# Kernel tuning notes

Measured on AMD Instinct MI355X. Metric: run time of the kernel, lower is better.

Reference implementation:

```python
import jax, jax.numpy as jnp
import numpy as np

B, N, K, NS = 2, 1024, 64, 32          # batch, points, keypoints (top-k), ball-query neighbors
RADIUS = 1.0                            # ball-query radius (sample_and_group)
R_VOX, S_VOX = 2.0, 0.4                 # voxelize search radius / step
NV = int(round(2 * R_VOX / S_VOX)) + 1  # 11 offsets per axis
C = NV ** 3                             # 1331 candidates per keypoint
F = 32                                  # deep feature channels (num_feat)


def _gather(data, idx):
    # data: (B, N, ...) ; idx: (B, ...) int -> (B, idx_shape..., ...)
    return jax.vmap(lambda d, i: d[i])(data, idx)


def setup_inputs() -> dict:
    key = jax.random.key(0)
    ks = jax.random.split(key, 16)
    f = lambda k, s: jax.random.normal(k, s, dtype=jnp.float32)
    return {
        "src_pts": f(ks[0], (B, 6, N)),
        "tgt_pts": f(ks[1], (B, 6, N)),
        "R_init": f(ks[2], (1, 3, 3)),
        "t_init": f(ks[3], (3, 1)),
        # feature-extraction shared MLP (6 -> 32 -> 32)
        "W1": f(ks[4], (6, F)) * 0.4, "b1": jnp.zeros((F,), jnp.float32),
        "W2": f(ks[5], (F, F)) * 0.2, "b2": jnp.zeros((F,), jnp.float32),
        # weighting (saliency) MLP (32 -> 16 -> 1)
        "Ww1": f(ks[6], (F, 16)) * 0.3, "bw1": jnp.zeros((16,), jnp.float32),
        "Ww2": f(ks[7], (16, 1)) * 0.3, "bw2": jnp.zeros((1,), jnp.float32),
        # deep-feature-embedding shared MLP (3+32 -> 32 -> 32)
        "Wd1": f(ks[8], (3 + F, F)) * 0.3, "bd1": jnp.zeros((F,), jnp.float32),
        "Wd2": f(ks[9], (F, F)) * 0.2, "bd2": jnp.zeros((F,), jnp.float32),
    }


def reference(src_pts, tgt_pts, R_init, t_init,
              W1, b1, W2, b2, Ww1, bw1, Ww2, bw2, Wd1, bd1, Wd2, bd2):
    def fe(pts):                                   # shared feature extraction (FE1)
        x = jnp.transpose(pts, (0, 2, 1))          # (B,N,6)
        h = jax.nn.relu(x @ W1 + b1)
        return x[..., :3], jax.nn.relu(h @ W2 + b2)  # xyz (B,N,3), feat (B,N,F)

    def dfe(x):                                    # shared DFE mini-PointNet MLP
        h = jax.nn.relu(x @ Wd1 + bd1)
        return jax.nn.relu(h @ Wd2 + bd2)

    src_xyz_all, src_feat = fe(src_pts)
    tgt_xyz_all, tgt_feat = fe(tgt_pts)

    # ---- weighting layer: per-point saliency, top-K keypoints ----
    score = (jax.nn.relu(src_feat @ Ww1 + bw1) @ Ww2 + bw2)[..., 0]  # (B,N)
    _, key_idx = jax.lax.top_k(score, K)                              # (B,K)

    src_pts_T = jnp.transpose(src_pts, (0, 2, 1))                     # (B,N,6)
    keypts = _gather(src_pts_T, key_idx)                              # (B,K,6)
    kxyz = keypts[..., :3]                                            # (B,K,3)

    # ---- sample_and_group: ball query among keypoints (npoint == K) ----
    sqd = jnp.sum((kxyz[:, :, None] - kxyz[:, None]) ** 2, -1)        # (B,K,K)
    gidx = jnp.broadcast_to(jnp.arange(K), (B, K, K))
    gidx = jnp.where(sqd > RADIUS ** 2, K, gidx)
    gidx = jnp.sort(gidx, -1)[:, :, :NS]
    gidx = jnp.where(gidx == K, gidx[:, :, :1], gidx)                 # (B,K,NS)

    grouped = _gather(kxyz, gidx)                                     # (B,K,NS,3)
    rel = grouped - kxyz[:, :, None]                                  # local coords
    orig_idx = _gather(key_idx, gidx)                                 # (B,K,NS) into N
    keyfeats = _gather(src_feat, orig_idx)                            # (B,K,NS,F)
    src_cat = jnp.concatenate([rel, keyfeats], -1)                    # (B,K,NS,3+F)

    # ---- voxelize: candidate grid around R_init-transformed keypoints ----
    Rm = jnp.broadcast_to(R_init, (B, 3, 3))
    kxyz_t = jnp.einsum('bij,bkj->bki', Rm, kxyz)                     # (B,K,3)
    off = jnp.linspace(-R_VOX, R_VOX, NV, dtype=jnp.float32)
    gx, gy, gz = jnp.meshgrid(off, off, off, indexing='ij')
    grid = jnp.stack([gx, gy, gz], -1).reshape(-1, 3)                 # (C,3)
    cand = kxyz_t[:, :, None, :] + grid                               # (B,K,C,3)

    # ---- 1-NN of each candidate in the target cloud (feature lookup) ----
    cn = jnp.sum(cand ** 2, -1)                                       # (B,K,C)
    tn = jnp.sum(tgt_xyz_all ** 2, -1)                                # (B,N)
    cross = jnp.einsum('bkcd,bnd->bkcn', cand, tgt_xyz_all)           # (B,K,C,N)
    d = cn[..., None] + tn[:, None, None, :] - 2.0 * cross
    nn = jnp.argmin(jax.lax.stop_gradient(d), -1)                     # (B,K,C)
    nn_xyz = _gather(tgt_xyz_all, nn)                                 # (B,K,C,3)
    nn_feat = _gather(tgt_feat, nn)                                   # (B,K,C,F)
    tgt_cat = jnp.concatenate([cand - nn_xyz, nn_feat], -1)           # (B,K,C,3+F)

    # ---- DFE embeddings + corresponding-point generation (CPG) ----
    src_emb = jnp.max(dfe(src_cat), axis=2)                           # (B,K,F)  max over neighbors
    tgt_emb = dfe(tgt_cat)                                            # (B,K,C,F)
    sim = jnp.einsum('bkd,bkcd->bkc', src_emb, tgt_emb)               # (B,K,C)
    w = jax.nn.softmax(sim, -1)
    tgt_vcp = jnp.einsum('bkc,bkcd->bkd', w, cand)                    # (B,K,3)

    return kxyz, tgt_vcp
```

## Files before the change

kernel.cpp:

```cpp
#include <hip/hip_runtime.h>
#include <math.h>

#define BB 2
#define NPTS 1024
#define KK 64
#define NSZ 32
#define CC 1331
#define FF 32
#define RAD2 1.0f
#define NCOL 121
#define NRNG 8

__global__ __launch_bounds__(64)
void k_features(const float* __restrict__ src_pts, const float* __restrict__ tgt_pts,
                const float* __restrict__ W1, const float* __restrict__ b1,
                const float* __restrict__ W2, const float* __restrict__ b2,
                const float* __restrict__ Ww1, const float* __restrict__ bw1,
                const float* __restrict__ Ww2, const float* __restrict__ bw2,
                const float* __restrict__ Wd1, const float* __restrict__ bd1,
                float* __restrict__ src_feat, float* __restrict__ tgt_A,
                float* __restrict__ tgt_m2, float* __restrict__ score)
{
    int gid = blockIdx.x * blockDim.x + threadIdx.x;
    int isTgt = gid >= BB * NPTS;
    int pn = gid & (BB * NPTS - 1);
    int b = pn >> 10, n = pn & 1023;
    const float* pts = isTgt ? tgt_pts : src_pts;
    float p[6];
#pragma unroll
    for (int i = 0; i < 6; i++) p[i] = pts[(b * 6 + i) * NPTS + n];
    float h[FF];
#pragma unroll
    for (int j = 0; j < FF; j++) {
        float a = b1[j];
#pragma unroll
        for (int i = 0; i < 6; i++) a = fmaf(p[i], W1[i * FF + j], a);
        h[j] = fmaxf(a, 0.0f);
    }
    float ft[FF];
#pragma unroll
    for (int j = 0; j < FF; j++) {
        float a = b2[j];
#pragma unroll
        for (int i = 0; i < FF; i++) a = fmaf(h[i], W2[i * FF + j], a);
        ft[j] = fmaxf(a, 0.0f);
    }
    if (isTgt) {
        float x = p[0], y = p[1], z = p[2];
        float4 v; v.x = x; v.y = y; v.z = z; v.w = x * x + y * y + z * z;
        ((float4*)tgt_m2)[b * NPTS + n] = v;
        float av[FF];
#pragma unroll
        for (int j = 0; j < FF; j++) av[j] = bd1[j];
#pragma unroll
        for (int i = 0; i < FF; i++) {
            float fi = ft[i];
#pragma unroll
            for (int j = 0; j < FF; j++)
                av[j] = fmaf(fi, Wd1[(3 + i) * FF + j], av[j]);
        }
#pragma unroll
        for (int j = 0; j < FF; j++) tgt_A[(b * NPTS + n) * FF + j] = av[j];
    } else {
#pragma unroll
        for (int j = 0; j < FF; j++) src_feat[(b * NPTS + n) * FF + j] = ft[j];
        float acc = bw2[0];
#pragma unroll
        for (int j = 0; j < 16; j++) {
            float a = bw1[j];
#pragma unroll
            for (int i = 0; i < FF; i++) a = fmaf(ft[i], Ww1[i * 16 + j], a);
            acc = fmaf(fmaxf(a, 0.0f), Ww2[j], acc);
        }
        score[b * NPTS + n] = acc;
    }
}

__global__ __launch_bounds__(256)
void k_rank(const float* __restrict__ score, const float* __restrict__ src_pts,
            const float* __restrict__ R,
            int* __restrict__ key_idx, float* __restrict__ kxyz,
            float* __restrict__ kxyz_t, float* __restrict__ out_kxyz)
{
    int blk = blockIdx.x;
    int b = blk >> 4;
    int pbase = (blk & 15) << 6;
    int t = threadIdx.x;
    int sub = t & 3;
    int lp = t >> 2;
    int n = pbase + lp;
    __shared__ float sc[NPTS];
    for (int i = t; i < NPTS; i += 256) sc[i] = score[b * NPTS + i];
    __syncthreads();
    float s = sc[n];
    int rank = 0;
#pragma unroll 8
    for (int jj = 0; jj < 256; jj++) {
        int j = (jj << 2) | sub;
        float sj = sc[j];
        bool before = (sj > s) || (sj == s && j < n);
        rank += before ? 1 : 0;
    }
    rank += __shfl_xor(rank, 1, 64);
    rank += __shfl_xor(rank, 2, 64);
    if (sub == 0 && rank < KK) {
        key_idx[b * KK + rank] = n;
        float x = src_pts[(b * 6 + 0) * NPTS + n];
        float y = src_pts[(b * 6 + 1) * NPTS + n];
        float z = src_pts[(b * 6 + 2) * NPTS + n];
        int o = (b * KK + rank) * 3;
        kxyz[o] = x; kxyz[o + 1] = y; kxyz[o + 2] = z;
        out_kxyz[o] = x; out_kxyz[o + 1] = y; out_kxyz[o + 2] = z;
#pragma unroll
        for (int i = 0; i < 3; i++)
            kxyz_t[o + i] = R[i * 3 + 0] * x + R[i * 3 + 1] * y + R[i * 3 + 2] * z;
    }
}

__global__ __launch_bounds__(64)
void k_group_emb(const float* __restrict__ kxyz, const int* __restrict__ key_idx,
                 const float* __restrict__ src_feat,
                 const float* __restrict__ Wd1, const float* __restrict__ bd1,
                 const float* __restrict__ Wd2, const float* __restrict__ bd2,
                 float* __restrict__ src_emb)
{
    int b = blockIdx.x / KK, kk = blockIdx.x % KK;
    int t = threadIdx.x;
    __shared__ float kx[KK][3];
    __shared__ float emb[NSZ][FF];
    kx[t][0] = kxyz[(b * KK + t) * 3 + 0];
    kx[t][1] = kxyz[(b * KK + t) * 3 + 1];
    kx[t][2] = kxyz[(b * KK + t) * 3 + 2];
    __syncthreads();
    float cx = kx[kk][0], cy = kx[kk][1], cz = kx[kk][2];
    float dx = kx[t][0] - cx, dy = kx[t][1] - cy, dz = kx[t][2] - cz;
    float sq = dx * dx + dy * dy + dz * dz;
    unsigned long long mask = __ballot(sq <= RAD2);
    if (t < NSZ) {
        int cnt = __popcll(mask);
        int want = (t < cnt) ? t : 0;
        unsigned long long mm = mask;
        for (int q = 0; q < want; q++) mm &= (mm - 1);
        int g = __ffsll(mm) - 1;
        float xr = kx[g][0] - cx, yr = kx[g][1] - cy, zr = kx[g][2] - cz;
        int orig = key_idx[b * KK + g];
        const float* fz = &src_feat[(b * NPTS + orig) * FF];
        float fr[FF];
#pragma unroll
        for (int i = 0; i < FF; i++) fr[i] = fz[i];
        float h[FF];
#pragma unroll
        for (int j = 0; j < FF; j++) {
            float a = bd1[j];
            a = fmaf(xr, Wd1[0 * FF + j], a);
            a = fmaf(yr, Wd1[1 * FF + j], a);
            a = fmaf(zr, Wd1[2 * FF + j], a);
#pragma unroll
            for (int i = 0; i < FF; i++) a = fmaf(fr[i], Wd1[(3 + i) * FF + j], a);
            h[j] = fmaxf(a, 0.0f);
        }
#pragma unroll
        for (int j = 0; j < FF; j++) {
            float a = bd2[j];
#pragma unroll
            for (int i = 0; i < FF; i++) a = fmaf(h[i], Wd2[i * FF + j], a);
            emb[t][j] = fmaxf(a, 0.0f);
        }
    }
    __syncthreads();
    if (t < FF) {
        float m = emb[0][t];
#pragma unroll
        for (int s2 = 1; s2 < NSZ; s2++) m = fmaxf(m, emb[s2][t]);
        src_emb[(b * KK + kk) * FF + t] = m;
    }
}

__global__ __launch_bounds__(256)
void k_scan(const float* __restrict__ kxyz_t, const float* __restrict__ tgt_m2,
            float2* __restrict__ part)
{
    int bid = blockIdx.x;
    int bk = bid >> 3, r = bid & 7;
    int b = bk >> 6;
    int t = threadIdx.x;
    int u = t >> 7, lt = t & 127;
    __shared__ float4 P[128];
    __shared__ float2 pbuf[2][NCOL][11];
    if (t < 128) P[t] = ((const float4*)tgt_m2)[(b << 10) + (r << 7) + t];
    float kx = kxyz_t[bk * 3 + 0], ky = kxyz_t[bk * 3 + 1], kz = kxyz_t[bk * 3 + 2];
    float kx2 = -2.0f * kx, ky2 = -2.0f * ky, kz2 = -2.0f * kz;
    int p = lt;
    bool active = p < NCOL;
    int pc = active ? p : 0;
    int ixv = pc / 11, iyv = pc - ixv * 11;
    float gx2 = -2.0f * (-2.0f + ixv * 0.4f);
    float gy2 = -2.0f * (-2.0f + iyv * 0.4f);
    float gz2[11];
#pragma unroll
    for (int iz = 0; iz < 11; iz++) gz2[iz] = -2.0f * (-2.0f + iz * 0.4f);
    float best[11]; int bn[11];
#pragma unroll
    for (int iz = 0; iz < 11; iz++) { best[iz] = 3.0e38f; bn[iz] = 0; }
    __syncthreads();
    if (active) {
        const int pb = u << 6;
#pragma unroll 8
        for (int i = 0; i < 64; i++) {
            float4 v = P[pb + i];
            float a = fmaf(kx2, v.x, fmaf(ky2, v.y, fmaf(kz2, v.z, v.w)));
            float e = fmaf(gx2, v.x, fmaf(gy2, v.y, a));
#pragma unroll
            for (int iz = 0; iz < 11; iz++) {
                float d = fmaf(gz2[iz], v.z, e);
                bool l = d < best[iz];
                best[iz] = l ? d : best[iz];
                bn[iz] = l ? i : bn[iz];
            }
        }
#pragma unroll
        for (int iz = 0; iz < 11; iz++)
            pbuf[u][p][iz] = make_float2(best[iz], __int_as_float(bn[iz] + (u << 6)));
    }
    __syncthreads();
    if (u == 0 && active) {
        int cbase = ((bk << 3) + r) * CC + p * 11;
#pragma unroll
        for (int iz = 0; iz < 11; iz++) {
            float2 r0 = pbuf[0][p][iz], r1 = pbuf[1][p][iz];
            float2 m = (r1.x < r0.x) ? r1 : r0;
            part[cbase + iz] = make_float2(m.x,
                __int_as_float(__float_as_int(m.y) + (r << 7)));
        }
    }
}

__global__ __launch_bounds__(256)
void k_mlp(const float2* __restrict__ part, const float* __restrict__ kxyz_t,
           const float* __restrict__ tgt_m2, const float* __restrict__ tgt_A,
           const float* __restrict__ src_emb,
           const float* __restrict__ Wd1,
           const float* __restrict__ Wd2, const float* __restrict__ bd2,
           float* __restrict__ sim)
{
    const int NCH = 6;
    int bid = blockIdx.x;
    int chunk = bid % NCH;
    int bk = bid / NCH;
    int b = bk >> 6;
    int t = threadIdx.x;
    int c = chunk * 256 + t;
    int cc = min(c, CC - 1);
    float2 rb = part[(bk << 3) * CC + cc];
#pragma unroll
    for (int r = 1; r < NRNG; r++) {
        float2 o = part[((bk << 3) + r) * CC + cc];
        if (o.x < rb.x) rb = o;
    }
    int nb = __float_as_int(rb.y);
    float4 nv = ((const float4*)tgt_m2)[(b << 10) + nb];
    const float4* az = (const float4*)&tgt_A[((b << 10) + nb) * FF];
    float h[FF];
#pragma unroll
    for (int i = 0; i < FF / 4; i++) {
        float4 v = az[i];
        h[i * 4 + 0] = v.x; h[i * 4 + 1] = v.y; h[i * 4 + 2] = v.z; h[i * 4 + 3] = v.w;
    }
    int ixv = cc / 121, rem = cc - ixv * 121, iyv = rem / 11, izv = rem - iyv * 11;
    float cx = kxyz_t[bk * 3 + 0] + (-2.0f + ixv * 0.4f);
    float cy = kxyz_t[bk * 3 + 1] + (-2.0f + iyv * 0.4f);
    float cz = kxyz_t[bk * 3 + 2] + (-2.0f + izv * 0.4f);
    float x0 = cx - nv.x, x1 = cy - nv.y, x2 = cz - nv.z;
#pragma unroll
    for (int j = 0; j < FF; j++) {
        float a = h[j];
        a = fmaf(x0, Wd1[0 * FF + j], a);
        a = fmaf(x1, Wd1[1 * FF + j], a);
        a = fmaf(x2, Wd1[2 * FF + j], a);
        h[j] = fmaxf(a, 0.0f);
    }
    float sv = 0.0f;
#pragma unroll
    for (int j = 0; j < FF; j++) {
        float a = bd2[j];
#pragma unroll
        for (int i = 0; i < FF; i++) a = fmaf(h[i], Wd2[i * FF + j], a);
        sv = fmaf(fmaxf(a, 0.0f), src_emb[bk * FF + j], sv);
    }
    if (c < CC) sim[bk * CC + c] = sv;
}

__global__ __launch_bounds__(256)
void k_softmax(const float* __restrict__ sim, const float* __restrict__ kxyz_t,
               float* __restrict__ out_vcp)
{
    int bk = blockIdx.x;
    int t = threadIdx.x;
    __shared__ float red[256];
    __shared__ float4 red4[256];
    float kx = kxyz_t[bk * 3 + 0], ky = kxyz_t[bk * 3 + 1], kz = kxyz_t[bk * 3 + 2];
    float lm = -3.0e38f;
    for (int c = t; c < CC; c += 256) lm = fmaxf(lm, sim[bk * CC + c]);
    red[t] = lm;
    __syncthreads();
    for (int s2 = 128; s2 > 0; s2 >>= 1) {
        if (t < s2) red[t] = fmaxf(red[t], red[t + s2]);
        __syncthreads();
    }
    float m = red[0];
    float se = 0.f, sx = 0.f, sy = 0.f, sz = 0.f;
    for (int c = t; c < CC; c += 256) {
        float e = expf(sim[bk * CC + c] - m);
        int ix = c / 121, rem = c - ix * 121, iy = rem / 11, iz = rem - iy * 11;
        float cxx = kx + (-2.0f + ix * 0.4f);
        float cyy = ky + (-2.0f + iy * 0.4f);
        float czz = kz + (-2.0f + iz * 0.4f);
        se += e;
        sx = fmaf(e, cxx, sx);
        sy = fmaf(e, cyy, sy);
        sz = fmaf(e, czz, sz);
    }
    red4[t] = make_float4(se, sx, sy, sz);
    __syncthreads();
    for (int s2 = 128; s2 > 0; s2 >>= 1) {
        if (t < s2) {
            float4 a = red4[t], bq = red4[t + s2];
            red4[t] = make_float4(a.x + bq.x, a.y + bq.y, a.z + bq.z, a.w + bq.w);
        }
        __syncthreads();
    }
    if (t == 0) {
        float4 r = red4[0];
        out_vcp[bk * 3 + 0] = r.y / r.x;
        out_vcp[bk * 3 + 1] = r.z / r.x;
        out_vcp[bk * 3 + 2] = r.w / r.x;
    }
}

extern "C" void kernel_launch(void* const* d_in, const int* in_sizes, int n_in,
                              void* d_out, int out_size, void* d_ws, size_t ws_size,
                              hipStream_t stream)
{
    (void)in_sizes; (void)n_in; (void)out_size; (void)ws_size;
    const float* src_pts = (const float*)d_in[0];
    const float* tgt_pts = (const float*)d_in[1];
    const float* R_init  = (const float*)d_in[2];
    const float* W1  = (const float*)d_in[4];
    const float* b1  = (const float*)d_in[5];
    const float* W2  = (const float*)d_in[6];
    const float* b2  = (const float*)d_in[7];
    const float* Ww1 = (const float*)d_in[8];
    const float* bw1 = (const float*)d_in[9];
    const float* Ww2 = (const float*)d_in[10];
    const float* bw2 = (const float*)d_in[11];
    const float* Wd1 = (const float*)d_in[12];
    const float* bd1 = (const float*)d_in[13];
    const float* Wd2 = (const float*)d_in[14];
    const float* bd2 = (const float*)d_in[15];

    float* ws = (float*)d_ws;
    float* src_feat = ws;
    float* tgt_A    = src_feat + BB * NPTS * FF;
    float* tgt_m2   = tgt_A + BB * NPTS * FF;
    float* score    = tgt_m2 + BB * NPTS * 4;
    int*   key_idx  = (int*)(score + BB * NPTS);
    float* kxyz     = (float*)(key_idx + BB * KK);
    float* kxyz_t   = kxyz + BB * KK * 3;
    float* src_emb  = kxyz_t + BB * KK * 3;
    float* sim      = src_emb + BB * KK * FF;
    float2* part    = (float2*)(sim + BB * KK * CC);

    float* out_kxyz = (float*)d_out;
    float* out_vcp  = out_kxyz + BB * KK * 3;

    k_features<<<64, 64, 0, stream>>>(
        src_pts, tgt_pts, W1, b1, W2, b2, Ww1, bw1, Ww2, bw2, Wd1, bd1,
        src_feat, tgt_A, tgt_m2, score);
    k_rank<<<BB * 16, 256, 0, stream>>>(score, src_pts, R_init,
                                        key_idx, kxyz, kxyz_t, out_kxyz);
    k_group_emb<<<BB * KK, 64, 0, stream>>>(kxyz, key_idx, src_feat,
                                            Wd1, bd1, Wd2, bd2, src_emb);
    k_scan<<<BB * KK * NRNG, 256, 0, stream>>>(kxyz_t, tgt_m2, part);
    k_mlp<<<BB * KK * 6, 256, 0, stream>>>(part, kxyz_t, tgt_m2, tgt_A, src_emb,
                                           Wd1, Wd2, bd2, sim);
    k_softmax<<<BB * KK, 256, 0, stream>>>(sim, kxyz_t, out_vcp);
}
```

Baseline: 74.97 us.

## Fuse all stages into one persistent kernel with global atomic barriers

Replaces six kernel launches with a single 256-block persistent kernel that runs each stage in turn, separated by atomic-counter grid barriers. The barrier counter is reset with a memset before launch. The goal is to remove per-launch overhead and the gaps between the small dependent kernels. The scan stage is also reorganised: each block now handles half the target ranges in four passes over 32-point subchunks. In exchange the code relies on all 256 blocks being resident at the same time, adds spin-wait barrier cost, and leaves most blocks idle in the small stages.

```diff
diff --git a/kernel.cpp b/kernel.cpp
--- a/kernel.cpp
+++ b/kernel.cpp
@@ -10,330 +10,340 @@
 #define RAD2 1.0f
 #define NCOL 121
 #define NRNG 8
-
-__global__ __launch_bounds__(64)
-void k_features(const float* __restrict__ src_pts, const float* __restrict__ tgt_pts,
-                const float* __restrict__ W1, const float* __restrict__ b1,
-                const float* __restrict__ W2, const float* __restrict__ b2,
-                const float* __restrict__ Ww1, const float* __restrict__ bw1,
-                const float* __restrict__ Ww2, const float* __restrict__ bw2,
-                const float* __restrict__ Wd1, const float* __restrict__ bd1,
-                float* __restrict__ src_feat, float* __restrict__ tgt_A,
-                float* __restrict__ tgt_m2, float* __restrict__ score)
+#define NBLK 256
+#define NTHR 512
+
+__device__ __forceinline__ void gbar(unsigned* bar, int id) {
+    __syncthreads();
+    if (threadIdx.x == 0) {
+        __threadfence();
+        __hip_atomic_fetch_add(&bar[id], 1u, __ATOMIC_ACQ_REL, __HIP_MEMORY_SCOPE_AGENT);
+        while (__hip_atomic_load(&bar[id], __ATOMIC_ACQUIRE, __HIP_MEMORY_SCOPE_AGENT) < NBLK) {
+            __builtin_amdgcn_s_sleep(8);
+        }
+        __threadfence();
+    }
+    __syncthreads();
+}
+
+__global__ __launch_bounds__(NTHR, 2)
+void k_all(const float* __restrict__ src_pts, const float* __restrict__ tgt_pts,
+           const float* __restrict__ R,
+           const float* __restrict__ W1, const float* __restrict__ b1,
+           const float* __restrict__ W2, const float* __restrict__ b2,
+           const float* __restrict__ Ww1, const float* __restrict__ bw1,
+           const float* __restrict__ Ww2, const float* __restrict__ bw2,
+           const float* __restrict__ Wd1, const float* __restrict__ bd1,
+           const float* __restrict__ Wd2, const float* __restrict__ bd2,
+           float* src_feat, float* tgt_A, float* tgt_m2, float* score,
+           int* key_idx, float* kxyz, float* kxyz_t, float* src_emb,
+           float* sim, float2* part, unsigned* bar,
+           float* out_kxyz, float* out_vcp)
 {
-    int gid = blockIdx.x * blockDim.x + threadIdx.x;
-    int isTgt = gid >= BB * NPTS;
-    int pn = gid & (BB * NPTS - 1);
-    int b = pn >> 10, n = pn & 1023;
-    const float* pts = isTgt ? tgt_pts : src_pts;
-    float p[6];
-#pragma unroll
-    for (int i = 0; i < 6; i++) p[i] = pts[(b * 6 + i) * NPTS + n];
-    float h[FF];
-#pragma unroll
-    for (int j = 0; j < FF; j++) {
-        float a = b1[j];
-#pragma unroll
-        for (int i = 0; i < 6; i++) a = fmaf(p[i], W1[i * FF + j], a);
-        h[j] = fmaxf(a, 0.0f);
-    }
-    float ft[FF];
-#pragma unroll
-    for (int j = 0; j < FF; j++) {
-        float a = b2[j];
-#pragma unroll
-        for (int i = 0; i < FF; i++) a = fmaf(h[i], W2[i * FF + j], a);
-        ft[j] = fmaxf(a, 0.0f);
-    }
-    if (isTgt) {
-        float x = p[0], y = p[1], z = p[2];
-        float4 v; v.x = x; v.y = y; v.z = z; v.w = x * x + y * y + z * z;
-        ((float4*)tgt_m2)[b * NPTS + n] = v;
-        float av[FF];
-#pragma unroll
-        for (int j = 0; j < FF; j++) av[j] = bd1[j];
-#pragma unroll
-        for (int i = 0; i < FF; i++) {
-            float fi = ft[i];
-#pragma unroll
-            for (int j = 0; j < FF; j++)
-                av[j] = fmaf(fi, Wd1[(3 + i) * FF + j], av[j]);
-        }
-#pragma unroll
-        for (int j = 0; j < FF; j++) tgt_A[(b * NPTS + n) * FF + j] = av[j];
-    } else {
-#pragma unroll
-        for (int j = 0; j < FF; j++) src_feat[(b * NPTS + n) * FF + j] = ft[j];
-        float acc = bw2[0];
-#pragma unroll
-        for (int j = 0; j < 16; j++) {
-            float a = bw1[j];
-#pragma unroll
-            for (int i = 0; i < FF; i++) a = fmaf(ft[i], Ww1[i * 16 + j], a);
-            acc = fmaf(fmaxf(a, 0.0f), Ww2[j], acc);
-        }
-        score[b * NPTS + n] = acc;
-    }
-}
-
-__global__ __launch_bounds__(256)
-void k_rank(const float* __restrict__ score, const float* __restrict__ src_pts,
-            const float* __restrict__ R,
-            int* __restrict__ key_idx, float* __restrict__ kxyz,
-            float* __restrict__ kxyz_t, float* __restrict__ out_kxyz)
-{
-    int blk = blockIdx.x;
-    int b = blk >> 4;
-    int pbase = (blk & 15) << 6;
-    int t = threadIdx.x;
-    int sub = t & 3;
-    int lp = t >> 2;
-    int n = pbase + lp;
+    const int bid = blockIdx.x;
+    const int t = threadIdx.x;
+    __shared__ float4 P[128];
+    __shared__ float2 pbuf[4][NCOL][11];
     __shared__ float sc[NPTS];
-    for (int i = t; i < NPTS; i += 256) sc[i] = score[b * NPTS + i];
-    __syncthreads();
-    float s = sc[n];
-    int rank = 0;
+    __shared__ float kxs[KK][3];
+    __shared__ float embs[NSZ][FF];
+    __shared__ float red[NTHR];
+    __shared__ float4 red4[NTHR];
+
+    {
+        int gid = bid * NTHR + t;
+        if (gid < 2 * BB * NPTS) {
+            int isTgt = gid >= BB * NPTS;
+            int pn = gid & (BB * NPTS - 1);
+            int b = pn >> 10, n = pn & 1023;
+            const float* pts = isTgt ? tgt_pts : src_pts;
+            float p[6];
+#pragma unroll
+            for (int i = 0; i < 6; i++) p[i] = pts[(b * 6 + i) * NPTS + n];
+            float h[FF];
+#pragma unroll
+            for (int j = 0; j < FF; j++) {
+                float a = b1[j];
+#pragma unroll
+                for (int i = 0; i < 6; i++) a = fmaf(p[i], W1[i * FF + j], a);
+                h[j] = fmaxf(a, 0.0f);
+            }
+            float ft[FF];
+#pragma unroll
+            for (int j = 0; j < FF; j++) {
+                float a = b2[j];
+#pragma unroll
+                for (int i = 0; i < FF; i++) a = fmaf(h[i], W2[i * FF + j], a);
+                ft[j] = fmaxf(a, 0.0f);
+            }
+            if (isTgt) {
+                float x = p[0], y = p[1], z = p[2];
+                float4 v; v.x = x; v.y = y; v.z = z; v.w = x * x + y * y + z * z;
+                ((float4*)tgt_m2)[b * NPTS + n] = v;
+                float av[FF];
+#pragma unroll
+                for (int j = 0; j < FF; j++) av[j] = bd1[j];
+#pragma unroll
+                for (int i = 0; i < FF; i++) {
+                    float fi = ft[i];
+#pragma unroll
+                    for (int j = 0; j < FF; j++)
+                        av[j] = fmaf(fi, Wd1[(3 + i) * FF + j], av[j]);
+                }
+#pragma unroll
+                for (int j = 0; j < FF; j++) tgt_A[(b * NPTS + n) * FF + j] = av[j];
+            } else {
+#pragma unroll
+                for (int j = 0; j < FF; j++) src_feat[(b * NPTS + n) * FF + j] = ft[j];
+                float acc = bw2[0];
+#pragma unroll
+                for (int j = 0; j < 16; j++) {
+                    float a = bw1[j];
+#pragma unroll
+                    for (int i = 0; i < FF; i++) a = fmaf(ft[i], Ww1[i * 16 + j], a);
+                    acc = fmaf(fmaxf(a, 0.0f), Ww2[j], acc);
+                }
+                score[b * NPTS + n] = acc;
+            }
+        }
+    }
+    gbar(bar, 0);
+
+    if (bid < BB * 16) {
+        int b = bid >> 4;
+        int pbase = (bid & 15) << 6;
+        for (int i = t; i < NPTS; i += NTHR) sc[i] = score[b * NPTS + i];
+        __syncthreads();
+        if (t < 256) {
+            int sub = t & 3;
+            int lp = t >> 2;
+            int n = pbase + lp;
+            float s = sc[n];
+            int rank = 0;
 #pragma unroll 8
-    for (int jj = 0; jj < 256; jj++) {
-        int j = (jj << 2) | sub;
-        float sj = sc[j];
-        bool before = (sj > s) || (sj == s && j < n);
-        rank += before ? 1 : 0;
-    }
-    rank += __shfl_xor(rank, 1, 64);
-    rank += __shfl_xor(rank, 2, 64);
-    if (sub == 0 && rank < KK) {
-        key_idx[b * KK + rank] = n;
-        float x = src_pts[(b * 6 + 0) * NPTS + n];
-        float y = src_pts[(b * 6 + 1) * NPTS + n];
-        float z = src_pts[(b * 6 + 2) * NPTS + n];
-        int o = (b * KK + rank) * 3;
-        kxyz[o] = x; kxyz[o + 1] = y; kxyz[o + 2] = z;
-        out_kxyz[o] = x; out_kxyz[o + 1] = y; out_kxyz[o + 2] = z;
-#pragma unroll
-        for (int i = 0; i < 3; i++)
-            kxyz_t[o + i] = R[i * 3 + 0] * x + R[i * 3 + 1] * y + R[i * 3 + 2] * z;
-    }
-}
-
-__global__ __launch_bounds__(64)
-void k_group_emb(const float* __restrict__ kxyz, const int* __restrict__ key_idx,
-                 const float* __restrict__ src_feat,
-                 const float* __restrict__ Wd1, const float* __restrict__ bd1,
-                 const float* __restrict__ Wd2, const float* __restrict__ bd2,
-                 float* __restrict__ src_emb)
-{
-    int b = blockIdx.x / KK, kk = blockIdx.x % KK;
-    int t = threadIdx.x;
-    __shared__ float kx[KK][3];
-    __shared__ float emb[NSZ][FF];
-    kx[t][0] = kxyz[(b * KK + t) * 3 + 0];
-    kx[t][1] = kxyz[(b * KK + t) * 3 + 1];
-    kx[t][2] = kxyz[(b * KK + t) * 3 + 2];
-    __syncthreads();
-    float cx = kx[kk][0], cy = kx[kk][1], cz = kx[kk][2];
-    float dx = kx[t][0] - cx, dy = kx[t][1] - cy, dz = kx[t][2] - cz;
-    float sq = dx * dx + dy * dy + dz * dz;
-    unsigned long long mask = __ballot(sq <= RAD2);
-    if (t < NSZ) {
-        int cnt = __popcll(mask);
-        int want = (t < cnt) ? t : 0;
-        unsigned long long mm = mask;
-        for (int q = 0; q < want; q++) mm &= (mm - 1);
-        int g = __ffsll(mm) - 1;
-        float xr = kx[g][0] - cx, yr = kx[g][1] - cy, zr = kx[g][2] - cz;
-        int orig = key_idx[b * KK + g];
-        const float* fz = &src_feat[(b * NPTS + orig) * FF];
-        float fr[FF];
-#pragma unroll
-        for (int i = 0; i < FF; i++) fr[i] = fz[i];
-        float h[FF];
-#pragma unroll
-        for (int j = 0; j < FF; j++) {
-            float a = bd1[j];
-            a = fmaf(xr, Wd1[0 * FF + j], a);
-            a = fmaf(yr, Wd1[1 * FF + j], a);
-            a = fmaf(zr, Wd1[2 * FF + j], a);
-#pragma unroll
-            for (int i = 0; i < FF; i++) a = fmaf(fr[i], Wd1[(3 + i) * FF + j], a);
-            h[j] = fmaxf(a, 0.0f);
-        }
-#pragma unroll
-        for (int j = 0; j < FF; j++) {
-            float a = bd2[j];
-#pragma unroll
-            for (int i = 0; i < FF; i++) a = fmaf(h[i], Wd2[i * FF + j], a);
-            emb[t][j] = fmaxf(a, 0.0f);
-        }
-    }
-    __syncthreads();
-    if (t < FF) {
-        float m = emb[0][t];
-#pragma unroll
-        for (int s2 = 1; s2 < NSZ; s2++) m = fmaxf(m, emb[s2][t]);
-        src_emb[(b * KK + kk) * FF + t] = m;
-    }
-}
-
-__global__ __launch_bounds__(256)
-void k_scan(const float* __restrict__ kxyz_t, const float* __restrict__ tgt_m2,
-            float2* __restrict__ part)
-{
-    int bid = blockIdx.x;
-    int bk = bid >> 3, r = bid & 7;
-    int b = bk >> 6;
-    int t = threadIdx.x;
-    int u = t >> 7, lt = t & 127;
-    __shared__ float4 P[128];
-    __shared__ float2 pbuf[2][NCOL][11];
-    if (t < 128) P[t] = ((const float4*)tgt_m2)[(b << 10) + (r << 7) + t];
-    float kx = kxyz_t[bk * 3 + 0], ky = kxyz_t[bk * 3 + 1], kz = kxyz_t[bk * 3 + 2];
-    float kx2 = -2.0f * kx, ky2 = -2.0f * ky, kz2 = -2.0f * kz;
-    int p = lt;
-    bool active = p < NCOL;
-    int pc = active ? p : 0;
-    int ixv = pc / 11, iyv = pc - ixv * 11;
-    float gx2 = -2.0f * (-2.0f + ixv * 0.4f);
-    float gy2 = -2.0f * (-2.0f + iyv * 0.4f);
-    float gz2[11];
-#pragma unroll
-    for (int iz = 0; iz < 11; iz++) gz2[iz] = -2.0f * (-2.0f + iz * 0.4f);
-    float best[11]; int bn[11];
-#pragma unroll
-    for (int iz = 0; iz < 11; iz++) { best[iz] = 3.0e38f; bn[iz] = 0; }
-    __syncthreads();
-    if (active) {
-        const int pb = u << 6;
+            for (int jj = 0; jj < 256; jj++) {
+                int j = (jj << 2) | sub;
+                float sj = sc[j];
+                bool before = (sj > s) || (sj == s && j < n);
+                rank += before ? 1 : 0;
+            }
+            rank += __shfl_xor(rank, 1, 64);
+            rank += __shfl_xor(rank, 2, 64);
+            if (sub == 0 && rank < KK) {
+                key_idx[b * KK + rank] = n;
+                float x = src_pts[(b * 6 + 0) * NPTS + n];
+                float y = src_pts[(b * 6 + 1) * NPTS + n];
+                float z = src_pts[(b * 6 + 2) * NPTS + n];
+                int o = (b * KK + rank) * 3;
+                kxyz[o] = x; kxyz[o + 1] = y; kxyz[o + 2] = z;
+                out_kxyz[o] = x; out_kxyz[o + 1] = y; out_kxyz[o + 2] = z;
+#pragma unroll
+                for (int i = 0; i < 3; i++)
+                    kxyz_t[o + i] = R[i * 3 + 0] * x + R[i * 3 + 1] * y + R[i * 3 + 2] * z;
+            }
+        }
+    }
+    gbar(bar, 1);
+
+    {
+        int bk = bid >> 1, half = bid & 1;
+        int b = bk >> 6;
+        int u = t >> 7, lt = t & 127;
+        float kx = kxyz_t[bk * 3 + 0], ky = kxyz_t[bk * 3 + 1], kz = kxyz_t[bk * 3 + 2];
+        float kx2 = -2.0f * kx, ky2 = -2.0f * ky, kz2 = -2.0f * kz;
+        bool active = lt < NCOL;
+        int pc = active ? lt : 0;
+        int ixv = pc / 11, iyv = pc - ixv * 11;
+        float gx2 = -2.0f * (-2.0f + ixv * 0.4f);
+        float gy2 = -2.0f * (-2.0f + iyv * 0.4f);
+        float gz2[11];
+#pragma unroll
+        for (int iz = 0; iz < 11; iz++) gz2[iz] = -2.0f * (-2.0f + iz * 0.4f);
+        for (int pass = 0; pass < 4; pass++) {
+            int rr = half * 4 + pass;
+            if (t < 128) P[t] = ((const float4*)tgt_m2)[(b << 10) + (rr << 7) + t];
+            __syncthreads();
+            if (active) {
+                float best[11]; int bn[11];
+#pragma unroll
+                for (int iz = 0; iz < 11; iz++) { best[iz] = 3.0e38f; bn[iz] = 0; }
+                const int pb = u << 5;
 #pragma unroll 8
-        for (int i = 0; i < 64; i++) {
-            float4 v = P[pb + i];
-            float a = fmaf(kx2, v.x, fmaf(ky2, v.y, fmaf(kz2, v.z, v.w)));
-            float e = fmaf(gx2, v.x, fmaf(gy2, v.y, a));
-#pragma unroll
-            for (int iz = 0; iz < 11; iz++) {
-                float d = fmaf(gz2[iz], v.z, e);
-                bool l = d < best[iz];
-                best[iz] = l ? d : best[iz];
-                bn[iz] = l ? i : bn[iz];
-            }
-        }
-#pragma unroll
-        for (int iz = 0; iz < 11; iz++)
-            pbuf[u][p][iz] = make_float2(best[iz], __int_as_float(bn[iz] + (u << 6)));
-    }
-    __syncthreads();
-    if (u == 0 && active) {
-        int cbase = ((bk << 3) + r) * CC + p * 11;
-#pragma unroll
-        for (int iz = 0; iz < 11; iz++) {
-            float2 r0 = pbuf[0][p][iz], r1 = pbuf[1][p][iz];
-            float2 m = (r1.x < r0.x) ? r1 : r0;
-            part[cbase + iz] = make_float2(m.x,
-                __int_as_float(__float_as_int(m.y) + (r << 7)));
-        }
-    }
-}
-
-__global__ __launch_bounds__(256)
-void k_mlp(const float2* __restrict__ part, const float* __restrict__ kxyz_t,
-           const float* __restrict__ tgt_m2, const float* __restrict__ tgt_A,
-           const float* __restrict__ src_emb,
-           const float* __restrict__ Wd1,
-           const float* __restrict__ Wd2, const float* __restrict__ bd2,
-           float* __restrict__ sim)
-{
-    const int NCH = 6;
-    int bid = blockIdx.x;
-    int chunk = bid % NCH;
-    int bk = bid / NCH;
-    int b = bk >> 6;
-    int t = threadIdx.x;
-    int c = chunk * 256 + t;
-    int cc = min(c, CC - 1);
-    float2 rb = part[(bk << 3) * CC + cc];
-#pragma unroll
-    for (int r = 1; r < NRNG; r++) {
-        float2 o = part[((bk << 3) + r) * CC + cc];
-        if (o.x < rb.x) rb = o;
-    }
-    int nb = __float_as_int(rb.y);
-    float4 nv = ((const float4*)tgt_m2)[(b << 10) + nb];
-    const float4* az = (const float4*)&tgt_A[((b << 10) + nb) * FF];
-    float h[FF];
-#pragma unroll
-    for (int i = 0; i < FF / 4; i++) {
-        float4 v = az[i];
-        h[i * 4 + 0] = v.x; h[i * 4 + 1] = v.y; h[i * 4 + 2] = v.z; h[i * 4 + 3] = v.w;
-    }
-    int ixv = cc / 121, rem = cc - ixv * 121, iyv = rem / 11, izv = rem - iyv * 11;
-    float cx = kxyz_t[bk * 3 + 0] + (-2.0f + ixv * 0.4f);
-    float cy = kxyz_t[bk * 3 + 1] + (-2.0f + iyv * 0.4f);
-    float cz = kxyz_t[bk * 3 + 2] + (-2.0f + izv * 0.4f);
-    float x0 = cx - nv.x, x1 = cy - nv.y, x2 = cz - nv.z;
-#pragma unroll
-    for (int j = 0; j < FF; j++) {
-        float a = h[j];
-        a = fmaf(x0, Wd1[0 * FF + j], a);
-        a = fmaf(x1, Wd1[1 * FF + j], a);
-        a = fmaf(x2, Wd1[2 * FF + j], a);
-        h[j] = fmaxf(a, 0.0f);
-    }
-    float sv = 0.0f;
-#pragma unroll
-    for (int j = 0; j < FF; j++) {
-        float a = bd2[j];
-#pragma unroll
-        for (int i = 0; i < FF; i++) a = fmaf(h[i], Wd2[i * FF + j], a);
-        sv = fmaf(fmaxf(a, 0.0f), src_emb[bk * FF + j], sv);
-    }
-    if (c < CC) sim[bk * CC + c] = sv;
-}
-
-__global__ __launch_bounds__(256)
-void k_softmax(const float* __restrict__ sim, const float* __restrict__ kxyz_t,
-               float* __restrict__ out_vcp)
-{
-    int bk = blockIdx.x;
-    int t = threadIdx.x;
-    __shared__ float red[256];
-    __shared__ float4 red4[256];
-    float kx = kxyz_t[bk * 3 + 0], ky = kxyz_t[bk * 3 + 1], kz = kxyz_t[bk * 3 + 2];
-    float lm = -3.0e38f;
-    for (int c = t; c < CC; c += 256) lm = fmaxf(lm, sim[bk * CC + c]);
-    red[t] = lm;
-    __syncthreads();
-    for (int s2 = 128; s2 > 0; s2 >>= 1) {
-        if (t < s2) red[t] = fmaxf(red[t], red[t + s2]);
-        __syncthreads();
-    }
-    float m = red[0];
-    float se = 0.f, sx = 0.f, sy = 0.f, sz = 0.f;
-    for (int c = t; c < CC; c += 256) {
-        float e = expf(sim[bk * CC + c] - m);
-        int ix = c / 121, rem = c - ix * 121, iy = rem / 11, iz = rem - iy * 11;
-        float cxx = kx + (-2.0f + ix * 0.4f);
-        float cyy = ky + (-2.0f + iy * 0.4f);
-        float czz = kz + (-2.0f + iz * 0.4f);
-        se += e;
-        sx = fmaf(e, cxx, sx);
-        sy = fmaf(e, cyy, sy);
-        sz = fmaf(e, czz, sz);
-    }
-    red4[t] = make_float4(se, sx, sy, sz);
-    __syncthreads();
-    for (int s2 = 128; s2 > 0; s2 >>= 1) {
-        if (t < s2) {
-            float4 a = red4[t], bq = red4[t + s2];
-            red4[t] = make_float4(a.x + bq.x, a.y + bq.y, a.z + bq.z, a.w + bq.w);
-        }
-        __syncthreads();
-    }
-    if (t == 0) {
-        float4 r = red4[0];
-        out_vcp[bk * 3 + 0] = r.y / r.x;
-        out_vcp[bk * 3 + 1] = r.z / r.x;
-        out_vcp[bk * 3 + 2] = r.w / r.x;
+                for (int i = 0; i < 32; i++) {
+                    float4 v = P[pb + i];
+                    float a = fmaf(kx2, v.x, fmaf(ky2, v.y, fmaf(kz2, v.z, v.w)));
+                    float e = fmaf(gx2, v.x, fmaf(gy2, v.y, a));
+#pragma unroll
+                    for (int iz = 0; iz < 11; iz++) {
+                        float d = fmaf(gz2[iz], v.z, e);
+                        bool l = d < best[iz];
+                        best[iz] = l ? d : best[iz];
+                        bn[iz] = l ? i : bn[iz];
+                    }
+                }
+#pragma unroll
+                for (int iz = 0; iz < 11; iz++)
+                    pbuf[u][lt][iz] = make_float2(best[iz],
+                        __int_as_float(bn[iz] + (u << 5)));
+            }
+            __syncthreads();
+            for (int ci = t; ci < CC; ci += NTHR) {
+                int p = ci / 11, iz = ci - p * 11;
+                float2 m = pbuf[0][p][iz];
+#pragma unroll
+                for (int u2 = 1; u2 < 4; u2++) {
+                    float2 o = pbuf[u2][p][iz];
+                    if (o.x < m.x) m = o;
+                }
+                part[((bk << 3) + rr) * CC + ci] = make_float2(m.x,
+                    __int_as_float(__float_as_int(m.y) + (rr << 7)));
+            }
+            __syncthreads();
+        }
+    }
+    if (bid < BB * KK) {
+        int b = bid >> 6, kk = bid & 63;
+        if (t < KK) {
+            kxs[t][0] = kxyz[(b * KK + t) * 3 + 0];
+            kxs[t][1] = kxyz[(b * KK + t) * 3 + 1];
+            kxs[t][2] = kxyz[(b * KK + t) * 3 + 2];
+        }
+        __syncthreads();
+        if (t < KK) {
+            float cx = kxs[kk][0], cy = kxs[kk][1], cz = kxs[kk][2];
+            float dx = kxs[t][0] - cx, dy = kxs[t][1] - cy, dz = kxs[t][2] - cz;
+            float sq = dx * dx + dy * dy + dz * dz;
+            unsigned long long mask = __ballot(sq <= RAD2);
+            if (t < NSZ) {
+                int cnt = __popcll(mask);
+                int want = (t < cnt) ? t : 0;
+                unsigned long long mm = mask;
+                for (int q = 0; q < want; q++) mm &= (mm - 1);
+                int g = __ffsll(mm) - 1;
+                float xr = kxs[g][0] - cx, yr = kxs[g][1] - cy, zr = kxs[g][2] - cz;
+                int orig = key_idx[b * KK + g];
+                const float* fz = &src_feat[(b * NPTS + orig) * FF];
+                float fr[FF];
+#pragma unroll
+                for (int i = 0; i < FF; i++) fr[i] = fz[i];
+                float h[FF];
+#pragma unroll
+                for (int j = 0; j < FF; j++) {
+                    float a = bd1[j];
+                    a = fmaf(xr, Wd1[0 * FF + j], a);
+                    a = fmaf(yr, Wd1[1 * FF + j], a);
+                    a = fmaf(zr, Wd1[2 * FF + j], a);
+#pragma unroll
+                    for (int i = 0; i < FF; i++) a = fmaf(fr[i], Wd1[(3 + i) * FF + j], a);
+                    h[j] = fmaxf(a, 0.0f);
+                }
+#pragma unroll
+                for (int j = 0; j < FF; j++) {
+                    float a = bd2[j];
+#pragma unroll
+                    for (int i = 0; i < FF; i++) a = fmaf(h[i], Wd2[i * FF + j], a);
+                    embs[t][j] = fmaxf(a, 0.0f);
+                }
+            }
+        }
+        __syncthreads();
+        if (t < FF) {
+            float m = embs[0][t];
+#pragma unroll
+            for (int s2 = 1; s2 < NSZ; s2++) m = fmaxf(m, embs[s2][t]);
+            src_emb[(b * KK + kk) * FF + t] = m;
+        }
+    }
+    gbar(bar, 2);
+
+#pragma unroll
+    for (int pass = 0; pass < 2; pass++) {
+        int ci = pass * (NBLK * NTHR) + bid * NTHR + t;
+        if (ci < BB * KK * CC) {
+            int bk = ci / CC;
+            int c = ci - bk * CC;
+            int b = bk >> 6;
+            float2 rb = part[(bk << 3) * CC + c];
+#pragma unroll
+            for (int r = 1; r < NRNG; r++) {
+                float2 o = part[((bk << 3) + r) * CC + c];
+                if (o.x < rb.x) rb = o;
+            }
+            int nb = __float_as_int(rb.y);
+            float4 nv = ((const float4*)tgt_m2)[(b << 10) + nb];
+            const float4* az = (const float4*)&tgt_A[((b << 10) + nb) * FF];
+            float h[FF];
+#pragma unroll
+            for (int i = 0; i < FF / 4; i++) {
+                float4 v = az[i];
+                h[i * 4 + 0] = v.x; h[i * 4 + 1] = v.y;
+                h[i * 4 + 2] = v.z; h[i * 4 + 3] = v.w;
+            }
+            int ixv = c / 121, rem = c - ixv * 121, iyv = rem / 11, izv = rem - iyv * 11;
+            float cx = kxyz_t[bk * 3 + 0] + (-2.0f + ixv * 0.4f);
+            float cy = kxyz_t[bk * 3 + 1] + (-2.0f + iyv * 0.4f);
+            float cz = kxyz_t[bk * 3 + 2] + (-2.0f + izv * 0.4f);
+            float x0 = cx - nv.x, x1 = cy - nv.y, x2 = cz - nv.z;
+#pragma unroll
+            for (int j = 0; j < FF; j++) {
+                float a = h[j];
+                a = fmaf(x0, Wd1[0 * FF + j], a);
+                a = fmaf(x1, Wd1[1 * FF + j], a);
+                a = fmaf(x2, Wd1[2 * FF + j], a);
+                h[j] = fmaxf(a, 0.0f);
+            }
+            float sv = 0.0f;
+#pragma unroll
+            for (int j = 0; j < FF; j++) {
+                float a = bd2[j];
+#pragma unroll
+                for (int i = 0; i < FF; i++) a = fmaf(h[i], Wd2[i * FF + j], a);
+                sv = fmaf(fmaxf(a, 0.0f), src_emb[bk * FF + j], sv);
+            }
+            sim[bk * CC + c] = sv;
+        }
+    }
+    gbar(bar, 3);
+
+    if (bid < BB * KK) {
+        int bk = bid;
+        float kx = kxyz_t[bk * 3 + 0], ky = kxyz_t[bk * 3 + 1], kz = kxyz_t[bk * 3 + 2];
+        float lm = -3.0e38f;
+        for (int c = t; c < CC; c += NTHR) lm = fmaxf(lm, sim[bk * CC + c]);
+        red[t] = lm;
+        __syncthreads();
+        for (int s2 = NTHR / 2; s2 > 0; s2 >>= 1) {
+            if (t < s2) red[t] = fmaxf(red[t], red[t + s2]);
+            __syncthreads();
+        }
+        float m = red[0];
+        float se = 0.f, sx = 0.f, sy = 0.f, sz = 0.f;
+        for (int c = t; c < CC; c += NTHR) {
+            float e = expf(sim[bk * CC + c] - m);
+            int ix = c / 121, rem = c - ix * 121, iy = rem / 11, iz = rem - iy * 11;
+            float cxx = kx + (-2.0f + ix * 0.4f);
+            float cyy = ky + (-2.0f + iy * 0.4f);
+            float czz = kz + (-2.0f + iz * 0.4f);
+            se += e;
+            sx = fmaf(e, cxx, sx);
+            sy = fmaf(e, cyy, sy);
+            sz = fmaf(e, czz, sz);
+        }
+        red4[t] = make_float4(se, sx, sy, sz);
+        __syncthreads();
+        for (int s2 = NTHR / 2; s2 > 0; s2 >>= 1) {
+            if (t < s2) {
+                float4 a = red4[t], bq = red4[t + s2];
+                red4[t] = make_float4(a.x + bq.x, a.y + bq.y, a.z + bq.z, a.w + bq.w);
+            }
+            __syncthreads();
+        }
+        if (t == 0) {
+            float4 r = red4[0];
+            out_vcp[bk * 3 + 0] = r.y / r.x;
+            out_vcp[bk * 3 + 1] = r.z / r.x;
+            out_vcp[bk * 3 + 2] = r.w / r.x;
+        }
     }
 }
 
@@ -369,19 +379,15 @@
     float* src_emb  = kxyz_t + BB * KK * 3;
     float* sim      = src_emb + BB * KK * FF;
     float2* part    = (float2*)(sim + BB * KK * CC);
+    unsigned* bar   = (unsigned*)(part + BB * KK * NRNG * CC);
 
     float* out_kxyz = (float*)d_out;
     float* out_vcp  = out_kxyz + BB * KK * 3;
 
-    k_features<<<64, 64, 0, stream>>>(
-        src_pts, tgt_pts, W1, b1, W2, b2, Ww1, bw1, Ww2, bw2, Wd1, bd1,
-        src_feat, tgt_A, tgt_m2, score);
-    k_rank<<<BB * 16, 256, 0, stream>>>(score, src_pts, R_init,
-                                        key_idx, kxyz, kxyz_t, out_kxyz);
-    k_group_emb<<<BB * KK, 64, 0, stream>>>(kxyz, key_idx, src_feat,
-                                            Wd1, bd1, Wd2, bd2, src_emb);
-    k_scan<<<BB * KK * NRNG, 256, 0, stream>>>(kxyz_t, tgt_m2, part);
-    k_mlp<<<BB * KK * 6, 256, 0, stream>>>(part, kxyz_t, tgt_m2, tgt_A, src_emb,
-                                           Wd1, Wd2, bd2, sim);
-    k_softmax<<<BB * KK, 256, 0, stream>>>(sim, kxyz_t, out_vcp);
+    hipMemsetAsync(bar, 0, 64, stream);
+    k_all<<<NBLK, NTHR, 0, stream>>>(
+        src_pts, tgt_pts, R_init,
+        W1, b1, W2, b2, Ww1, bw1, Ww2, bw2, Wd1, bd1, Wd2, bd2,
+        src_feat, tgt_A, tgt_m2, score, key_idx, kxyz, kxyz_t, src_emb,
+        sim, part, bar, out_kxyz, out_vcp);
 }
```

After: 237.1 us. 3.16x slower.

## Merge nearest-neighbor partials with 64-bit atomicMin instead of per-range buffers

Applied to the files above, without the earlier changes.

The scan kernel no longer stages two half-block results in shared memory and writes eight per-range partial arrays. Each thread packs an order-preserving float distance with the global index into a 64-bit key and applies atomicMin to a single per-candidate slot, which the rank kernel initialises. The MLP kernel then reads one key instead of reducing eight partials. This removes a barrier and cuts global traffic, in exchange for about 16 atomic operations per candidate, with the contention that brings.

```diff
diff --git a/kernel.cpp b/kernel.cpp
--- a/kernel.cpp
+++ b/kernel.cpp
@@ -80,12 +80,16 @@
 void k_rank(const float* __restrict__ score, const float* __restrict__ src_pts,
             const float* __restrict__ R,
             int* __restrict__ key_idx, float* __restrict__ kxyz,
-            float* __restrict__ kxyz_t, float* __restrict__ out_kxyz)
+            float* __restrict__ kxyz_t, float* __restrict__ out_kxyz,
+            unsigned long long* __restrict__ nnkey)
 {
     int blk = blockIdx.x;
     int b = blk >> 4;
     int pbase = (blk & 15) << 6;
     int t = threadIdx.x;
+    int gid = blk * 256 + t;
+    for (int i = gid; i < BB * KK * CC; i += BB * 16 * 256)
+        nnkey[i] = 0xFFFFFFFFFFFFFFFFull;
     int sub = t & 3;
     int lp = t >> 2;
     int n = pbase + lp;
@@ -178,7 +182,7 @@
 
 __global__ __launch_bounds__(256)
 void k_scan(const float* __restrict__ kxyz_t, const float* __restrict__ tgt_m2,
-            float2* __restrict__ part)
+            unsigned long long* __restrict__ nnkey)
 {
     int bid = blockIdx.x;
     int bk = bid >> 3, r = bid & 7;
@@ -186,13 +190,11 @@
     int t = threadIdx.x;
     int u = t >> 7, lt = t & 127;
     __shared__ float4 P[128];
-    __shared__ float2 pbuf[2][NCOL][11];
     if (t < 128) P[t] = ((const float4*)tgt_m2)[(b << 10) + (r << 7) + t];
     float kx = kxyz_t[bk * 3 + 0], ky = kxyz_t[bk * 3 + 1], kz = kxyz_t[bk * 3 + 2];
     float kx2 = -2.0f * kx, ky2 = -2.0f * ky, kz2 = -2.0f * kz;
-    int p = lt;
-    bool active = p < NCOL;
-    int pc = active ? p : 0;
+    bool active = lt < NCOL;
+    int pc = active ? lt : 0;
     int ixv = pc / 11, iyv = pc - ixv * 11;
     float gx2 = -2.0f * (-2.0f + ixv * 0.4f);
     float gy2 = -2.0f * (-2.0f + iyv * 0.4f);
@@ -218,25 +220,20 @@
                 bn[iz] = l ? i : bn[iz];
             }
         }
-#pragma unroll
-        for (int iz = 0; iz < 11; iz++)
-            pbuf[u][p][iz] = make_float2(best[iz], __int_as_float(bn[iz] + (u << 6)));
-    }
-    __syncthreads();
-    if (u == 0 && active) {
-        int cbase = ((bk << 3) + r) * CC + p * 11;
+        unsigned long long* base = &nnkey[(unsigned)bk * CC + pc * 11];
 #pragma unroll
         for (int iz = 0; iz < 11; iz++) {
-            float2 r0 = pbuf[0][p][iz], r1 = pbuf[1][p][iz];
-            float2 m = (r1.x < r0.x) ? r1 : r0;
-            part[cbase + iz] = make_float2(m.x,
-                __int_as_float(__float_as_int(m.y) + (r << 7)));
+            unsigned bb2 = __float_as_uint(best[iz]);
+            unsigned m = ((unsigned)(((int)bb2) >> 31)) | 0x80000000u;
+            unsigned nglob = (unsigned)((r << 7) + (u << 6) + bn[iz]);
+            unsigned long long key = ((unsigned long long)(bb2 ^ m) << 32) | nglob;
+            atomicMin(&base[iz], key);
         }
     }
 }
 
 __global__ __launch_bounds__(256)
-void k_mlp(const float2* __restrict__ part, const float* __restrict__ kxyz_t,
+void k_mlp(const unsigned long long* __restrict__ nnkey, const float* __restrict__ kxyz_t,
            const float* __restrict__ tgt_m2, const float* __restrict__ tgt_A,
            const float* __restrict__ src_emb,
            const float* __restrict__ Wd1,
@@ -251,13 +248,7 @@
     int t = threadIdx.x;
     int c = chunk * 256 + t;
     int cc = min(c, CC - 1);
-    float2 rb = part[(bk << 3) * CC + cc];
-#pragma unroll
-    for (int r = 1; r < NRNG; r++) {
-        float2 o = part[((bk << 3) + r) * CC + cc];
-        if (o.x < rb.x) rb = o;
-    }
-    int nb = __float_as_int(rb.y);
+    int nb = (int)(unsigned)(nnkey[(unsigned)bk * CC + cc] & 0xFFFFFFFFull);
     float4 nv = ((const float4*)tgt_m2)[(b << 10) + nb];
     const float4* az = (const float4*)&tgt_A[((b << 10) + nb) * FF];
     float h[FF];
@@ -368,7 +359,7 @@
     float* kxyz_t   = kxyz + BB * KK * 3;
     float* src_emb  = kxyz_t + BB * KK * 3;
     float* sim      = src_emb + BB * KK * FF;
-    float2* part    = (float2*)(sim + BB * KK * CC);
+    unsigned long long* nnkey = (unsigned long long*)(sim + BB * KK * CC);
 
     float* out_kxyz = (float*)d_out;
     float* out_vcp  = out_kxyz + BB * KK * 3;
@@ -377,11 +368,11 @@
         src_pts, tgt_pts, W1, b1, W2, b2, Ww1, bw1, Ww2, bw2, Wd1, bd1,
         src_feat, tgt_A, tgt_m2, score);
     k_rank<<<BB * 16, 256, 0, stream>>>(score, src_pts, R_init,
-                                        key_idx, kxyz, kxyz_t, out_kxyz);
+                                        key_idx, kxyz, kxyz_t, out_kxyz, nnkey);
     k_group_emb<<<BB * KK, 64, 0, stream>>>(kxyz, key_idx, src_feat,
                                             Wd1, bd1, Wd2, bd2, src_emb);
-    k_scan<<<BB * KK * NRNG, 256, 0, stream>>>(kxyz_t, tgt_m2, part);
-    k_mlp<<<BB * KK * 6, 256, 0, stream>>>(part, kxyz_t, tgt_m2, tgt_A, src_emb,
+    k_scan<<<BB * KK * NRNG, 256, 0, stream>>>(kxyz_t, tgt_m2, nnkey);
+    k_mlp<<<BB * KK * 6, 256, 0, stream>>>(nnkey, kxyz_t, tgt_m2, tgt_A, src_emb,
                                            Wd1, Wd2, bd2, sim);
     k_softmax<<<BB * KK, 256, 0, stream>>>(sim, kxyz_t, out_vcp);
 }
```

Result: slower. 167.4 us (+123.2%).
